# Performance work log

Hardware: AMD Instinct MI355X
Metric: run time of the kernel (lower is better)

## Reference

```python
import jax, jax.numpy as jnp
import numpy as np

B, S, D, U = 32, 2048, 1024, 1024


def setup_inputs() -> dict:
    key = jax.random.key(0)
    ks = jax.random.split(key, 8)
    scale_in = 1.0 / np.sqrt(D)
    scale_u = 1.0 / np.sqrt(U)
    return {
        "query": jax.random.normal(ks[0], (B, D), dtype=jnp.float32),
        "values": jax.random.normal(ks[1], (B, S, D), dtype=jnp.float32),
        "W1": jax.random.normal(ks[2], (D, U), dtype=jnp.float32) * scale_in,
        "b1": jnp.zeros((U,), dtype=jnp.float32),
        "W2": jax.random.normal(ks[3], (D, U), dtype=jnp.float32) * scale_in,
        "b2": jnp.zeros((U,), dtype=jnp.float32),
        "V": jax.random.normal(ks[4], (U, 1), dtype=jnp.float32) * scale_u,
        "bV": jnp.zeros((1,), dtype=jnp.float32),
    }


def reference(query, values, W1, b1, W2, b2, V, bV):
    # values: [B, S, D] -> [B, S, U]; query: [B, D] -> [B, 1, U]
    proj_v = jnp.einsum("bsd,du->bsu", values, W1) + b1
    proj_q = (query @ W2 + b2)[:, None, :]
    # score: [B, S, 1]
    score = jnp.einsum("bsu,uo->bso", jnp.tanh(proj_v + proj_q), V) + bV
    attention_weights = jax.nn.softmax(score, axis=1)
    # context: [B, D]
    context_vector = jnp.sum(attention_weights * values, axis=1)
    return (context_vector, attention_weights)
```

## Files before the change

kernel.cpp:

```cpp
#include <hip/hip_runtime.h>

#define DEVFN __device__ __forceinline__

typedef __attribute__((ext_vector_type(4))) float f32x4;
typedef __attribute__((ext_vector_type(8))) short short8;
typedef __attribute__((ext_vector_type(4))) unsigned int uint4v;
typedef __attribute__((ext_vector_type(8))) unsigned short ushort8;

constexpr int CB = 32;
constexpr int CS = 2048;
constexpr int CD = 1024;
constexpr int CU = 1024;
constexpr int CM = CB * CS;

DEVFN unsigned f2bf_u(float f) {
    unsigned u = __float_as_uint(f);
    return (u + 0x7FFFu + ((u >> 16) & 1u)) >> 16;
}
DEVFN unsigned f2bf_pack(float lo, float hi) {
    return f2bf_u(lo) | (f2bf_u(hi) << 16);
}
DEVFN short8 cvt8(f32x4 a, f32x4 b) {
    uint4v p;
    p[0] = f2bf_pack(a[0], a[1]);
    p[1] = f2bf_pack(a[2], a[3]);
    p[2] = f2bf_pack(b[0], b[1]);
    p[3] = f2bf_pack(b[2], b[3]);
    return __builtin_bit_cast(short8, p);
}
DEVFN float tanh_fast(float x) {
    float e = exp2f(x * 2.885390081777927f);
    return 1.0f - 2.0f * __builtin_amdgcn_rcpf(e + 1.0f);
}

__global__ void k_bias1(const float* __restrict__ q, const float* __restrict__ W2,
                        float* __restrict__ bpart) {
    int dc = blockIdx.x, b = blockIdx.y;
    int t = threadIdx.x;
    __shared__ float qs[128];
    if (t < 128) qs[t] = q[b * CD + dc * 128 + t];
    __syncthreads();
    float acc0 = 0.f, acc1 = 0.f, acc2 = 0.f, acc3 = 0.f;
    const float* w2 = W2 + (size_t)(dc * 128) * CU + t;
#pragma unroll 4
    for (int d = 0; d < 128; ++d) {
        float qv = qs[d];
        const float* r = w2 + (size_t)d * CU;
        acc0 += qv * r[0];
        acc1 += qv * r[256];
        acc2 += qv * r[512];
        acc3 += qv * r[768];
    }
    float* o = bpart + (size_t)(b * 8 + dc) * CU + t;
    o[0] = acc0; o[256] = acc1; o[512] = acc2; o[768] = acc3;
}

__global__ void k_bias2(const float* __restrict__ bpart, const float* __restrict__ b1,
                        const float* __restrict__ b2, float* __restrict__ bias) {
    int idx = blockIdx.x * 256 + threadIdx.x;
    int b = idx >> 10, u = idx & 1023;
    float s = b1[u] + b2[u];
#pragma unroll
    for (int dc = 0; dc < 8; ++dc) s += bpart[(size_t)(b * 8 + dc) * CU + u];
    bias[idx] = s;
}

__global__ void k_packW1(const float* __restrict__ W1, unsigned short* __restrict__ W1p) {
    int tid = blockIdx.x * 256 + threadIdx.x;
    int o8  = tid * 8;
    int l   = (o8 >> 3) & 63;
    int ub  = (o8 >> 9) & 15;
    int ut  = (o8 >> 13) & 3;
    int kt  = o8 >> 15;
    int u  = ut * 256 + ub * 16 + (l & 15);
    int d0 = kt * 32 + (l >> 4) * 8;
    ushort8 v;
#pragma unroll
    for (int j = 0; j < 8; ++j)
        v[j] = (unsigned short)f2bf_u(W1[(size_t)(d0 + j) * CU + u]);
    *(ushort8*)(W1p + o8) = v;
}

__global__ __launch_bounds__(256, 2) void k_score(
    const float* __restrict__ values, const unsigned short* __restrict__ W1p,
    const float* __restrict__ bias, const float* __restrict__ V,
    float* __restrict__ score4) {
    __shared__ __align__(16) char smem[16384];

    const int t = threadIdx.x;
    const int w = t >> 6, l = t & 63;
    const int p = blockIdx.x;
    const int L = (p & 7) * 256 + (p >> 3);
    const int xt = L >> 2;
    const int uc = L & 3;
    const int ph = xt & 31;
    const int m0 = xt * 128;
    const int bb = m0 >> 11;

    const float* aSrc0 = values + (size_t)(m0 + (t >> 2)) * CD + (t & 3) * 8;
    const float* aSrc1 = aSrc0 + (size_t)64 * CD;
    const int hh = t & 3;
    const int aWr0 = w * 1024 + (((((t >> 2) & 15) ^ (hh << 2)) | (hh << 4)) << 4);
    const int aWr1 = aWr0 + 4096;
    const int hR = l >> 4;
    const int aRdOff = ((((l & 15) ^ (hR << 2)) | (hR << 4)) << 4);
    const unsigned short* bBase = W1p + (size_t)uc * 8192 + w * 2048 + l * 8;

    f32x4 acc[8][4];
#pragma unroll
    for (int i = 0; i < 8; ++i)
#pragma unroll
        for (int j = 0; j < 4; ++j) acc[i][j] = f32x4{0.f, 0.f, 0.f, 0.f};

    short8 bF0[4], bF1[4];
    f32x4 a0a, a0b, a1a, a1b;

    {
        const unsigned short* bs = bBase + (size_t)ph * 32768;
#pragma unroll
        for (int jj = 0; jj < 4; ++jj)
            bF0[jj] = *(const short8*)(bs + jj * 512);
        a0a = __builtin_nontemporal_load((const f32x4*)(aSrc0 + ph * 32));
        a0b = __builtin_nontemporal_load((const f32x4*)(aSrc0 + ph * 32 + 4));
        a1a = __builtin_nontemporal_load((const f32x4*)(aSrc1 + ph * 32));
        a1b = __builtin_nontemporal_load((const f32x4*)(aSrc1 + ph * 32 + 4));
        *(short8*)(smem + aWr0) = cvt8(a0a, a0b);
        *(short8*)(smem + aWr1) = cvt8(a1a, a1b);
        const int kp1 = (ph + 1) & 31;
        a0a = __builtin_nontemporal_load((const f32x4*)(aSrc0 + kp1 * 32));
        a0b = __builtin_nontemporal_load((const f32x4*)(aSrc0 + kp1 * 32 + 4));
        a1a = __builtin_nontemporal_load((const f32x4*)(aSrc1 + kp1 * 32));
        a1b = __builtin_nontemporal_load((const f32x4*)(aSrc1 + kp1 * 32 + 4));
        asm volatile("s_waitcnt lgkmcnt(0)" ::: "memory");
        asm volatile("s_barrier" ::: "memory");
    }

#define SCORE_BODY(KT, BF_CUR, BF_NXT, DO_WRB, DO_LDA)                              \
    {                                                                               \
        const char* aB = smem + ((KT) & 1) * 8192;                                  \
        short8 aF[8];                                                               \
        _Pragma("unroll")                                                           \
        for (int i = 0; i < 8; ++i)                                                 \
            aF[i] = *(const short8*)(aB + i * 1024 + aRdOff);                       \
        if (DO_WRB) {                                                               \
            char* wB = smem + (((KT) + 1) & 1) * 8192;                              \
            *(short8*)(wB + aWr0) = cvt8(a0a, a0b);                                 \
            *(short8*)(wB + aWr1) = cvt8(a1a, a1b);                                 \
            const int kp = ((KT) + 1 + ph) & 31;                                    \
            const unsigned short* bs = bBase + (size_t)kp * 32768;                  \
            _Pragma("unroll")                                                       \
            for (int jj = 0; jj < 4; ++jj)                                          \
                BF_NXT[jj] = *(const short8*)(bs + jj * 512);                       \
        }                                                                           \
        if (DO_LDA) {                                                               \
            const int kp = ((KT) + 2 + ph) & 31;                                    \
            a0a = __builtin_nontemporal_load((const f32x4*)(aSrc0 + kp * 32));      \
            a0b = __builtin_nontemporal_load((const f32x4*)(aSrc0 + kp * 32 + 4));  \
            a1a = __builtin_nontemporal_load((const f32x4*)(aSrc1 + kp * 32));      \
            a1b = __builtin_nontemporal_load((const f32x4*)(aSrc1 + kp * 32 + 4));  \
        }                                                                           \
        __builtin_amdgcn_s_setprio(1);                                              \
        _Pragma("unroll")                                                           \
        for (int i = 0; i < 8; ++i)                                                 \
            _Pragma("unroll")                                                       \
            for (int j = 0; j < 4; ++j)                                             \
                acc[i][j] = __builtin_amdgcn_mfma_f32_16x16x32_bf16(                \
                    aF[i], BF_CUR[j], acc[i][j], 0, 0, 0);                          \
        __builtin_amdgcn_s_setprio(0);                                              \
        asm volatile("s_waitcnt lgkmcnt(0)" ::: "memory");                          \
        asm volatile("s_barrier" ::: "memory");                                     \
    }

    for (int kt = 0; kt < 30; kt += 2) {
        SCORE_BODY(kt,     bF0, bF1, 1, 1)
        SCORE_BODY(kt + 1, bF1, bF0, 1, 1)
    }
    SCORE_BODY(30, bF0, bF1, 1, 0)
    SCORE_BODY(31, bF1, bF0, 0, 0)
#undef SCORE_BODY

    float part[8][4];
#pragma unroll
    for (int i = 0; i < 8; ++i)
#pragma unroll
        for (int rr = 0; rr < 4; ++rr) part[i][rr] = 0.f;

#pragma unroll
    for (int j = 0; j < 4; ++j) {
        const int col = uc * 256 + w * 64 + j * 16 + (l & 15);
        const float vv = V[col];
        const float bz = bias[bb * CU + col];
#pragma unroll
        for (int i = 0; i < 8; ++i)
#pragma unroll
            for (int rr = 0; rr < 4; ++rr)
                part[i][rr] += vv * tanh_fast(acc[i][j][rr] + bz);
    }

    float* red = (float*)smem;
#pragma unroll
    for (int i = 0; i < 8; ++i)
#pragma unroll
        for (int rr = 0; rr < 4; ++rr) {
            float v = part[i][rr];
            v += __shfl_xor(v, 1);
            v += __shfl_xor(v, 2);
            v += __shfl_xor(v, 4);
            v += __shfl_xor(v, 8);
            if ((l & 15) == 0)
                red[w * 128 + i * 16 + (l >> 4) * 4 + rr] = v;
        }
    __syncthreads();
    if (t < 128) {
        float sv = red[t] + red[128 + t] + red[256 + t] + red[384 + t];
        score4[(size_t)uc * CM + m0 + t] = sv;
    }
}

__global__ void k_softmax(const float* __restrict__ score4, float* __restrict__ wts) {
    int b = blockIdx.x, t = threadIdx.x;
    int i0 = b * CS + t, i1 = i0 + 1024;
    float s0 = score4[i0] + score4[CM + i0] + score4[2 * CM + i0] + score4[3 * CM + i0];
    float s1 = score4[i1] + score4[CM + i1] + score4[2 * CM + i1] + score4[3 * CM + i1];
    __shared__ float red[16];
    int wv = t >> 6, ln = t & 63;
    float m = fmaxf(s0, s1);
#pragma unroll
    for (int o = 32; o >= 1; o >>= 1) m = fmaxf(m, __shfl_xor(m, o));
    if (ln == 0) red[wv] = m;
    __syncthreads();
    float M = red[0];
#pragma unroll
    for (int k = 1; k < 16; ++k) M = fmaxf(M, red[k]);
    float e0 = __expf(s0 - M), e1 = __expf(s1 - M);
    float sm = e0 + e1;
#pragma unroll
    for (int o = 32; o >= 1; o >>= 1) sm += __shfl_xor(sm, o);
    __syncthreads();
    if (ln == 0) red[wv] = sm;
    __syncthreads();
    float T = 0.f;
#pragma unroll
    for (int k = 0; k < 16; ++k) T += red[k];
    float inv = 1.0f / T;
    wts[i0] = e0 * inv;
    wts[i1] = e1 * inv;
}

__global__ void k_ctx_part(const float* __restrict__ values, const float* __restrict__ wts,
                           float* __restrict__ part) {
    int b = blockIdx.y, sc = blockIdx.x;
    int t = threadIdx.x;
    const float* vb = values + ((size_t)b * CS + sc * 64) * CD + t * 4;
    const float* wb = wts + b * CS + sc * 64;
    f32x4 a = {0.f, 0.f, 0.f, 0.f};
#pragma unroll 8
    for (int s = 0; s < 64; ++s) {
        float wgt = wb[s];
        f32x4 v = *(const f32x4*)(vb + (size_t)s * CD);
        a += v * wgt;
    }
    *(f32x4*)(part + (size_t)(b * 32 + sc) * CD + t * 4) = a;
}

__global__ void k_ctx_red(const float* __restrict__ part, float* __restrict__ ctx) {
    int idx = blockIdx.x * 256 + threadIdx.x;
    int b = idx >> 10, d = idx & 1023;
    float s = 0.f;
#pragma unroll 8
    for (int c = 0; c < 32; ++c) s += part[(size_t)(b * 32 + c) * CD + d];
    ctx[idx] = s;
}

extern "C" void kernel_launch(void* const* d_in, const int* in_sizes, int n_in,
                              void* d_out, int out_size, void* d_ws, size_t ws_size,
                              hipStream_t stream) {
    const float* query  = (const float*)d_in[0];
    const float* values = (const float*)d_in[1];
    const float* W1     = (const float*)d_in[2];
    const float* b1     = (const float*)d_in[3];
    const float* W2     = (const float*)d_in[4];
    const float* b2     = (const float*)d_in[5];
    const float* V      = (const float*)d_in[6];

    float* out = (float*)d_out;
    float* ctx = out;
    float* wts = out + 32768;

    char* ws = (char*)d_ws;
    float*          score4 = (float*)ws;
    float*          bias   = (float*)(ws + (1 << 20));
    unsigned short* W1p    = (unsigned short*)(ws + (1 << 20) + (1 << 17));
    float*          part   = (float*)(ws + (1 << 20) + (1 << 17) + (1 << 21));
    float*          bpart  = part;

    k_bias1<<<dim3(8, 32), 256, 0, stream>>>(query, W2, bpart);
    k_bias2<<<128, 256, 0, stream>>>(bpart, b1, b2, bias);
    k_packW1<<<512, 256, 0, stream>>>(W1, W1p);
    k_score<<<2048, 256, 0, stream>>>(values, W1p, bias, V, score4);
    k_softmax<<<32, 1024, 0, stream>>>(score4, wts);
    k_ctx_part<<<dim3(32, 32), 256, 0, stream>>>(values, wts, part);
    k_ctx_red<<<128, 256, 0, stream>>>(part, ctx);
}
```

Measured before the change: 275.5 us.

## Switch score GEMM to 32x32x16 MFMA with triple-buffered LDS pipeline

Replaces the 16x16x32 bf16 MFMA tiling with 32x32x16 MFMAs, repacking W1 into a matching fragment layout and changing the A-tile LDS layout and swizzle. The LDS A buffer goes from double to triple buffering, so there is one barrier per k-step with a partial lgkmcnt wait instead of a full drain. The epilogue reduction is reworked for the 32-lane column groups. This aims to cut LDS read traffic per FLOP and barrier stalls, at the cost of more LDS, which may lower occupancy, and a more complex index mapping.

After: 274.5 us. No clear change (-0.4%).

```diff
diff --git a/kernel.cpp b/kernel.cpp
--- a/kernel.cpp
+++ b/kernel.cpp
@@ -3,6 +3,7 @@
 #define DEVFN __device__ __forceinline__
 
 typedef __attribute__((ext_vector_type(4))) float f32x4;
+typedef __attribute__((ext_vector_type(16))) float f32x16;
 typedef __attribute__((ext_vector_type(8))) short short8;
 typedef __attribute__((ext_vector_type(4))) unsigned int uint4v;
 typedef __attribute__((ext_vector_type(8))) unsigned short ushort8;
@@ -67,13 +68,14 @@
 
 __global__ void k_packW1(const float* __restrict__ W1, unsigned short* __restrict__ W1p) {
     int tid = blockIdx.x * 256 + threadIdx.x;
-    int o8  = tid * 8;
-    int l   = (o8 >> 3) & 63;
-    int ub  = (o8 >> 9) & 15;
-    int ut  = (o8 >> 13) & 3;
-    int kt  = o8 >> 15;
-    int u  = ut * 256 + ub * 16 + (l & 15);
-    int d0 = kt * 32 + (l >> 4) * 8;
+    int o8 = tid * 8;
+    int l = (o8 >> 3) & 63;
+    int fragidx = o8 >> 9;
+    int h  = fragidx & 1;
+    int cb = (fragidx >> 1) & 31;
+    int kt = fragidx >> 6;
+    int d0 = kt * 32 + h * 16 + (l >> 5) * 8;
+    int u  = cb * 32 + (l & 31);
     ushort8 v;
 #pragma unroll
     for (int j = 0; j < 8; ++j)
@@ -85,7 +87,7 @@
     const float* __restrict__ values, const unsigned short* __restrict__ W1p,
     const float* __restrict__ bias, const float* __restrict__ V,
     float* __restrict__ score4) {
-    __shared__ __align__(16) char smem[16384];
+    __shared__ __align__(16) char smem[24576];
 
     const int t = threadIdx.x;
     const int w = t >> 6, l = t & 63;
@@ -97,119 +99,124 @@
     const int m0 = xt * 128;
     const int bb = m0 >> 11;
 
-    const float* aSrc0 = values + (size_t)(m0 + (t >> 2)) * CD + (t & 3) * 8;
-    const float* aSrc1 = aSrc0 + (size_t)64 * CD;
-    const int hh = t & 3;
-    const int aWr0 = w * 1024 + (((((t >> 2) & 15) ^ (hh << 2)) | (hh << 4)) << 4);
-    const int aWr1 = aWr0 + 4096;
-    const int hR = l >> 4;
-    const int aRdOff = ((((l & 15) ^ (hR << 2)) | (hR << 4)) << 4);
-    const unsigned short* bBase = W1p + (size_t)uc * 8192 + w * 2048 + l * 8;
-
-    f32x4 acc[8][4];
-#pragma unroll
-    for (int i = 0; i < 8; ++i)
-#pragma unroll
-        for (int j = 0; j < 4; ++j) acc[i][j] = f32x4{0.f, 0.f, 0.f, 0.f};
+    const int sRow = t >> 1, sH = t & 1;
+    const float* aSrcT = values + (size_t)(m0 + sRow) * CD + sH * 16;
+    const int aWr = ((sRow >> 5) * 2 + sH) * 1024 + (((sRow & 31) ^ (sH << 1)) << 4);
+    const int aRd0 = l << 4;
+    const int aRd1 = (l ^ 2) << 4;
+    const unsigned short* bBase = W1p + (uc * 8 + w * 2) * 1024 + l * 8;
+
+    f32x16 acc[4][2];
+#pragma unroll
+    for (int i = 0; i < 4; ++i)
+#pragma unroll
+        for (int j = 0; j < 2; ++j)
+#pragma unroll
+            for (int r = 0; r < 16; ++r) acc[i][j][r] = 0.f;
 
     short8 bF0[4], bF1[4];
-    f32x4 a0a, a0b, a1a, a1b;
+    f32x4 hA0, hA1, hA2, hA3;
 
     {
         const unsigned short* bs = bBase + (size_t)ph * 32768;
 #pragma unroll
         for (int jj = 0; jj < 4; ++jj)
             bF0[jj] = *(const short8*)(bs + jj * 512);
-        a0a = __builtin_nontemporal_load((const f32x4*)(aSrc0 + ph * 32));
-        a0b = __builtin_nontemporal_load((const f32x4*)(aSrc0 + ph * 32 + 4));
-        a1a = __builtin_nontemporal_load((const f32x4*)(aSrc1 + ph * 32));
-        a1b = __builtin_nontemporal_load((const f32x4*)(aSrc1 + ph * 32 + 4));
-        *(short8*)(smem + aWr0) = cvt8(a0a, a0b);
-        *(short8*)(smem + aWr1) = cvt8(a1a, a1b);
+        const float* ap = aSrcT + ph * 32;
+        hA0 = *(const f32x4*)(ap);
+        hA1 = *(const f32x4*)(ap + 4);
+        hA2 = *(const f32x4*)(ap + 8);
+        hA3 = *(const f32x4*)(ap + 12);
+        *(short8*)(smem + aWr) = cvt8(hA0, hA1);
+        *(short8*)(smem + aWr + 512) = cvt8(hA2, hA3);
         const int kp1 = (ph + 1) & 31;
-        a0a = __builtin_nontemporal_load((const f32x4*)(aSrc0 + kp1 * 32));
-        a0b = __builtin_nontemporal_load((const f32x4*)(aSrc0 + kp1 * 32 + 4));
-        a1a = __builtin_nontemporal_load((const f32x4*)(aSrc1 + kp1 * 32));
-        a1b = __builtin_nontemporal_load((const f32x4*)(aSrc1 + kp1 * 32 + 4));
-        asm volatile("s_waitcnt lgkmcnt(0)" ::: "memory");
-        asm volatile("s_barrier" ::: "memory");
-    }
-
-#define SCORE_BODY(KT, BF_CUR, BF_NXT, DO_WRB, DO_LDA)                              \
+        const float* ap1 = aSrcT + kp1 * 32;
+        hA0 = *(const f32x4*)(ap1);
+        hA1 = *(const f32x4*)(ap1 + 4);
+        hA2 = *(const f32x4*)(ap1 + 8);
+        hA3 = *(const f32x4*)(ap1 + 12);
+    }
+
+#define SCORE_BODY(KT, RIDX, WIDX, BFC, BFN, DO_WR, DO_LDB, DO_LDA)                 \
     {                                                                               \
-        const char* aB = smem + ((KT) & 1) * 8192;                                  \
-        short8 aF[8];                                                               \
-        _Pragma("unroll")                                                           \
-        for (int i = 0; i < 8; ++i)                                                 \
-            aF[i] = *(const short8*)(aB + i * 1024 + aRdOff);                       \
-        if (DO_WRB) {                                                               \
-            char* wB = smem + (((KT) + 1) & 1) * 8192;                              \
-            *(short8*)(wB + aWr0) = cvt8(a0a, a0b);                                 \
-            *(short8*)(wB + aWr1) = cvt8(a1a, a1b);                                 \
+        if (DO_WR) {                                                                \
+            char* wB = smem + (WIDX) * 8192;                                        \
+            *(short8*)(wB + aWr) = cvt8(hA0, hA1);                                  \
+            *(short8*)(wB + aWr + 512) = cvt8(hA2, hA3);                            \
+        }                                                                           \
+        asm volatile("s_waitcnt lgkmcnt(2)" ::: "memory");                          \
+        asm volatile("s_barrier" ::: "memory");                                     \
+        if (DO_LDB) {                                                               \
             const int kp = ((KT) + 1 + ph) & 31;                                    \
             const unsigned short* bs = bBase + (size_t)kp * 32768;                  \
             _Pragma("unroll")                                                       \
             for (int jj = 0; jj < 4; ++jj)                                          \
-                BF_NXT[jj] = *(const short8*)(bs + jj * 512);                       \
+                BFN[jj] = *(const short8*)(bs + jj * 512);                          \
         }                                                                           \
         if (DO_LDA) {                                                               \
             const int kp = ((KT) + 2 + ph) & 31;                                    \
-            a0a = __builtin_nontemporal_load((const f32x4*)(aSrc0 + kp * 32));      \
-            a0b = __builtin_nontemporal_load((const f32x4*)(aSrc0 + kp * 32 + 4));  \
-            a1a = __builtin_nontemporal_load((const f32x4*)(aSrc1 + kp * 32));      \
-            a1b = __builtin_nontemporal_load((const f32x4*)(aSrc1 + kp * 32 + 4));  \
+            const float* ap = aSrcT + kp * 32;                                      \
+            hA0 = *(const f32x4*)(ap);                                              \
+            hA1 = *(const f32x4*)(ap + 4);                                          \
+            hA2 = *(const f32x4*)(ap + 8);                                          \
+            hA3 = *(const f32x4*)(ap + 12);                                         \
+        }                                                                           \
+        const char* aB = smem + (RIDX) * 8192;                                      \
+        short8 aF0[4], aF1[4];                                                      \
+        _Pragma("unroll")                                                           \
+        for (int rb = 0; rb < 4; ++rb) {                                            \
+            aF0[rb] = *(const short8*)(aB + (rb * 2) * 1024 + aRd0);                \
+            aF1[rb] = *(const short8*)(aB + (rb * 2 + 1) * 1024 + aRd1);            \
         }                                                                           \
         __builtin_amdgcn_s_setprio(1);                                              \
         _Pragma("unroll")                                                           \
-        for (int i = 0; i < 8; ++i)                                                 \
+        for (int rb = 0; rb < 4; ++rb)                                              \
             _Pragma("unroll")                                                       \
-            for (int j = 0; j < 4; ++j)                                             \
-                acc[i][j] = __builtin_amdgcn_mfma_f32_16x16x32_bf16(                \
-                    aF[i], BF_CUR[j], acc[i][j], 0, 0, 0);                          \
+            for (int cb = 0; cb < 2; ++cb)                                          \
+                acc[rb][cb] = __builtin_amdgcn_mfma_f32_32x32x16_bf16(              \
+                    aF0[rb], BFC[cb * 2], acc[rb][cb], 0, 0, 0);                    \
+        _Pragma("unroll")                                                           \
+        for (int rb = 0; rb < 4; ++rb)                                              \
+            _Pragma("unroll")                                                       \
+            for (int cb = 0; cb < 2; ++cb)                                          \
+                acc[rb][cb] = __builtin_amdgcn_mfma_f32_32x32x16_bf16(              \
+                    aF1[rb], BFC[cb * 2 + 1], acc[rb][cb], 0, 0, 0);                \
         __builtin_amdgcn_s_setprio(0);                                              \
-        asm volatile("s_waitcnt lgkmcnt(0)" ::: "memory");                          \
-        asm volatile("s_barrier" ::: "memory");                                     \
-    }
-
-    for (int kt = 0; kt < 30; kt += 2) {
-        SCORE_BODY(kt,     bF0, bF1, 1, 1)
-        SCORE_BODY(kt + 1, bF1, bF0, 1, 1)
-    }
-    SCORE_BODY(30, bF0, bF1, 1, 0)
-    SCORE_BODY(31, bF1, bF0, 0, 0)
+    }
+
+    for (int kt = 0; kt < 30; kt += 6) {
+        SCORE_BODY(kt + 0, 0, 1, bF0, bF1, 1, 1, 1)
+        SCORE_BODY(kt + 1, 1, 2, bF1, bF0, 1, 1, 1)
+        SCORE_BODY(kt + 2, 2, 0, bF0, bF1, 1, 1, 1)
+        SCORE_BODY(kt + 3, 0, 1, bF1, bF0, 1, 1, 1)
+        SCORE_BODY(kt + 4, 1, 2, bF0, bF1, 1, 1, (kt + 4 < 30))
+        SCORE_BODY(kt + 5, 2, 0, bF1, bF0, 1, 1, (kt + 5 < 30))
+    }
+    SCORE_BODY(30, 0, 1, bF0, bF1, 1, 1, 0)
+    SCORE_BODY(31, 1, 2, bF1, bF0, 0, 0, 0)
 #undef SCORE_BODY
 
-    float part[8][4];
-#pragma unroll
-    for (int i = 0; i < 8; ++i)
-#pragma unroll
-        for (int rr = 0; rr < 4; ++rr) part[i][rr] = 0.f;
-
-#pragma unroll
-    for (int j = 0; j < 4; ++j) {
-        const int col = uc * 256 + w * 64 + j * 16 + (l & 15);
-        const float vv = V[col];
-        const float bz = bias[bb * CU + col];
-#pragma unroll
-        for (int i = 0; i < 8; ++i)
-#pragma unroll
-            for (int rr = 0; rr < 4; ++rr)
-                part[i][rr] += vv * tanh_fast(acc[i][j][rr] + bz);
-    }
-
     float* red = (float*)smem;
-#pragma unroll
-    for (int i = 0; i < 8; ++i)
-#pragma unroll
-        for (int rr = 0; rr < 4; ++rr) {
-            float v = part[i][rr];
-            v += __shfl_xor(v, 1);
-            v += __shfl_xor(v, 2);
-            v += __shfl_xor(v, 4);
-            v += __shfl_xor(v, 8);
-            if ((l & 15) == 0)
-                red[w * 128 + i * 16 + (l >> 4) * 4 + rr] = v;
+    {
+        const int col0 = uc * 256 + w * 64 + (l & 31);
+        const float v0 = V[col0], v1 = V[col0 + 32];
+        const float z0 = bias[bb * CU + col0], z1 = bias[bb * CU + col0 + 32];
+#pragma unroll
+        for (int rb = 0; rb < 4; ++rb) {
+#pragma unroll
+            for (int r = 0; r < 16; ++r) {
+                float pv = v0 * tanh_fast(acc[rb][0][r] + z0)
+                         + v1 * tanh_fast(acc[rb][1][r] + z1);
+                pv += __shfl_xor(pv, 1);
+                pv += __shfl_xor(pv, 2);
+                pv += __shfl_xor(pv, 4);
+                pv += __shfl_xor(pv, 8);
+                pv += __shfl_xor(pv, 16);
+                if ((l & 31) == 0)
+                    red[w * 128 + rb * 32 + (r & 3) + 8 * (r >> 2) + 4 * (l >> 5)] = pv;
+            }
         }
+    }
     __syncthreads();
     if (t < 128) {
         float sv = red[t] + red[128 + t] + red[256 + t] + red[384 + t];
```
